# Performance work log

Hardware: AMD Instinct MI355X
Metric: run time of the kernel (lower is better)

The kernel has to match this reference:

```python
import jax, jax.numpy as jnp
import numpy as np

D = 128   # opt.geometric_latent_dim
H = 132   # FCBlock hidden width (hardcoded in source)
B = 65536
K = 8

def setup_inputs() -> dict:
    key = jax.random.key(0)
    ks = jax.random.split(key, 16)
    s = lambda k, shp, fan: jax.random.normal(k, shp, jnp.float32) / np.sqrt(fan)
    return {
        "signal": jax.random.normal(ks[0], (B, D), jnp.float32),
        "components": jax.random.normal(ks[1], (K, B, D), jnp.float32),
        # message_map / update_map: Linear(D, D)
        "Wm": s(ks[2], (D, D), D), "bm": jnp.zeros((D,), jnp.float32),
        "Wu": s(ks[3], (D, D), D), "bu": jnp.zeros((D,), jnp.float32),
        "W0": s(ks[4], (H, 2 * D), 2 * D), "b0": jnp.zeros((H,), jnp.float32),
        "W1": s(ks[5], (H, H), H),         "b1": jnp.zeros((H,), jnp.float32),
        "W2": s(ks[6], (H, H), H),         "b2": jnp.zeros((H,), jnp.float32),
        "W3": s(ks[7], (D, H), H),         "b3": jnp.zeros((D,), jnp.float32),
    }

def reference(signal, components, Wm, bm, Wu, bu, W0, b0, W1, b1, W2, b2, W3, b3):
    # message_map applied to each component, then summed over components
    msgs = jnp.einsum('kbd,ed->kbe', components, Wm) + bm  # [K,B,D]
    right = msgs.sum(axis=0)                               # [B,D]
    # update_map
    right = right @ Wu.T + bu                              # [B,D]
    # joint_update: FCBlock on concat([signal, right])
    x = jnp.concatenate([signal, right], axis=-1)          # [B,2D]
    x = jax.nn.relu(x @ W0.T + b0)
    x = jax.nn.relu(x @ W1.T + b1)
    x = jax.nn.relu(x @ W2.T + b2)
    return x @ W3.T + b3                                   # [B,D]
```

## Files before the change

### kernel.cpp

```cpp
#include <hip/hip_runtime.h>
#include <stdint.h>

#define DD  128
#define HH  132
#define BB  65536
#define KKC 8
#define HP  144
#define KP  160

typedef short bf16x8 __attribute__((ext_vector_type(8)));
typedef short bf16x4 __attribute__((ext_vector_type(4)));
typedef float f32x4  __attribute__((ext_vector_type(4)));

__device__ __forceinline__ unsigned short f2b(float f){
  union{float f; unsigned u;} c; c.f = f;
  unsigned r = c.u + 0x7fffu + ((c.u >> 16) & 1u);
  return (unsigned short)(r >> 16);
}

__global__ void prepA(const float* __restrict__ Wm, const float* __restrict__ bm,
                      const float* __restrict__ Wu, const float* __restrict__ bu,
                      float* __restrict__ Wf, float* __restrict__ bfv){
  int idx = blockIdx.x * 256 + threadIdx.x;
  int i = idx >> 7, j = idx & 127;
  float acc = 0.f;
  for(int d = 0; d < DD; ++d)
    acc += Wu[i*DD + d] * Wm[d*DD + j];
  Wf[idx] = acc;
  if(j == 0){
    float a = 0.f;
    for(int d = 0; d < DD; ++d) a += Wu[i*DD + d] * bm[d];
    bfv[i] = (float)KKC * a + bu[i];
  }
}

__global__ void prepB(const float* __restrict__ W0, const float* __restrict__ b0,
                      const float* __restrict__ W1, const float* __restrict__ b1,
                      const float* __restrict__ W2, const float* __restrict__ b2,
                      const float* __restrict__ W3, const float* __restrict__ b3,
                      const float* __restrict__ Wf, const float* __restrict__ bfv,
                      unsigned short* __restrict__ w0s_p, unsigned short* __restrict__ w0rp,
                      unsigned short* __restrict__ w1p,  unsigned short* __restrict__ w2p,
                      unsigned short* __restrict__ w3p,
                      float* __restrict__ b0p, float* __restrict__ b1p,
                      float* __restrict__ b2p, float* __restrict__ b3p){
  int idx = blockIdx.x * 256 + threadIdx.x;
  if(idx < HP*DD){
    int n = idx >> 7, k = idx & 127;
    w0s_p[idx] = (n < HH) ? f2b(W0[n*(2*DD) + k]) : (unsigned short)0;
    return;
  }
  idx -= HP*DD;
  if(idx < HP*DD){
    int n = idx >> 7, k = idx & 127;
    float acc = 0.f;
    if(n < HH)
      for(int i = 0; i < DD; ++i)
        acc += W0[n*(2*DD) + DD + i] * Wf[i*DD + k];
    w0rp[idx] = (n < HH) ? f2b(acc) : (unsigned short)0;
    return;
  }
  idx -= HP*DD;
  if(idx < HP*KP){
    int n = idx / KP, k = idx % KP;
    w1p[idx] = (n < HH && k < HH) ? f2b(W1[n*HH + k]) : (unsigned short)0;
    return;
  }
  idx -= HP*KP;
  if(idx < HP*KP){
    int n = idx / KP, k = idx % KP;
    w2p[idx] = (n < HH && k < HH) ? f2b(W2[n*HH + k]) : (unsigned short)0;
    return;
  }
  idx -= HP*KP;
  if(idx < DD*KP){
    int n = idx / KP, k = idx % KP;
    w3p[idx] = (k < HH) ? f2b(W3[n*HH + k]) : (unsigned short)0;
    return;
  }
  idx -= DD*KP;
  if(idx < HP){
    float acc = 0.f;
    if(idx < HH){
      acc = b0[idx];
      for(int i = 0; i < DD; ++i) acc += W0[idx*(2*DD) + DD + i] * bfv[i];
    }
    b0p[idx] = acc;
    return;
  }
  idx -= HP;
  if(idx < HP){ b1p[idx] = (idx < HH) ? b1[idx] : 0.f; return; }
  idx -= HP;
  if(idx < HP){ b2p[idx] = (idx < HH) ? b2[idx] : 0.f; return; }
  idx -= HP;
  if(idx < DD){ b3p[idx] = b3[idx]; return; }
}

__global__ __launch_bounds__(256) void comp_sum(
    const float* __restrict__ comps, unsigned short* __restrict__ sumb){
  const size_t base = (size_t)blockIdx.x * 8192;
  const int t = threadIdx.x;
  f32x4 acc[8];
  #pragma unroll
  for(int i = 0; i < 8; ++i) acc[i] = (f32x4){0.f,0.f,0.f,0.f};

  #pragma unroll
  for(int k = 0; k < KKC; ++k){
    const float* p = comps + (size_t)k * BB * DD + base + t*4;
    #pragma unroll
    for(int i = 0; i < 8; ++i){
      f32x4 v = *(const f32x4*)(p + i*1024);
      acc[i] += v;
    }
  }
  unsigned short* q = sumb + base + t*4;
  #pragma unroll
  for(int i = 0; i < 8; ++i){
    bf16x4 pk;
    #pragma unroll
    for(int j = 0; j < 4; ++j) pk[j] = (short)f2b(acc[i][j]);
    *(bf16x4*)(q + i*1024) = pk;
  }
}

__global__ __launch_bounds__(256) void fused_mlp(
    const float* __restrict__ signal,
    const unsigned short* __restrict__ sumb,
    const unsigned short* __restrict__ w0s_p,
    const unsigned short* __restrict__ w0rp,
    const unsigned short* __restrict__ w1p,
    const unsigned short* __restrict__ w2p,
    const unsigned short* __restrict__ w3p,
    const float* __restrict__ b0p, const float* __restrict__ b1p,
    const float* __restrict__ b2p, const float* __restrict__ b3p,
    float* __restrict__ out)
{
  const int tid  = threadIdx.x;
  const int lane = tid & 63;
  const int wave = tid >> 6;
  const int m    = lane & 15;
  const int quad = lane >> 4;
  const int rowBase = blockIdx.x * 64 + wave * 16;
  const int arow = rowBase + m;

  __shared__ unsigned short act[4][16][168];

  for(int t = tid; t < 4*16*16; t += 256){
    int wv = t >> 8, r = (t >> 4) & 15, c = t & 15;
    act[wv][r][144 + c] = 0;
  }
  __syncthreads();

  bf16x8 sumf[4];
  #pragma unroll
  for(int ki = 0; ki < 4; ++ki)
    sumf[ki] = *(const bf16x8*)(sumb + (size_t)arow*DD + ki*32 + quad*8);

  bf16x8 sigf[4];
  {
    const float* srow = signal + (size_t)arow * DD;
    #pragma unroll
    for(int ki = 0; ki < 4; ++ki){
      f32x4 lo = *(const f32x4*)(srow + ki*32 + quad*8);
      f32x4 hi = *(const f32x4*)(srow + ki*32 + quad*8 + 4);
      bf16x8 p;
      #pragma unroll
      for(int j = 0; j < 4; ++j){ p[j] = (short)f2b(lo[j]); p[4+j] = (short)f2b(hi[j]); }
      sigf[ki] = p;
    }
  }

  #pragma unroll
  for(int nt = 0; nt < 9; ++nt){
    f32x4 acc = {0.f,0.f,0.f,0.f};
    const unsigned short* wr1 = w0s_p + (size_t)(nt*16 + m)*DD + quad*8;
    const unsigned short* wr2 = w0rp  + (size_t)(nt*16 + m)*DD + quad*8;
    #pragma unroll
    for(int ki = 0; ki < 4; ++ki){
      bf16x8 wf = *(const bf16x8*)(wr1 + ki*32);
      acc = __builtin_amdgcn_mfma_f32_16x16x32_bf16(sigf[ki], wf, acc, 0, 0, 0);
    }
    #pragma unroll
    for(int ki = 0; ki < 4; ++ki){
      bf16x8 wf = *(const bf16x8*)(wr2 + ki*32);
      acc = __builtin_amdgcn_mfma_f32_16x16x32_bf16(sumf[ki], wf, acc, 0, 0, 0);
    }
    float bias = b0p[nt*16 + m];
    #pragma unroll
    for(int r = 0; r < 4; ++r){
      float v = acc[r] + bias;
      v = v > 0.f ? v : 0.f;
      act[wave][quad*4 + r][nt*16 + m] = f2b(v);
    }
  }
  __syncthreads();

  bf16x8 hf[5];

  #pragma unroll
  for(int ki = 0; ki < 5; ++ki)
    hf[ki] = *(const bf16x8*)&act[wave][m][ki*32 + quad*8];
  __syncthreads();
  #pragma unroll
  for(int nt = 0; nt < 9; ++nt){
    f32x4 acc = {0.f,0.f,0.f,0.f};
    const unsigned short* wr = w1p + (size_t)(nt*16 + m)*KP + quad*8;
    #pragma unroll
    for(int ki = 0; ki < 5; ++ki){
      bf16x8 wf = *(const bf16x8*)(wr + ki*32);
      acc = __builtin_amdgcn_mfma_f32_16x16x32_bf16(hf[ki], wf, acc, 0, 0, 0);
    }
    float bias = b1p[nt*16 + m];
    #pragma unroll
    for(int r = 0; r < 4; ++r){
      float v = acc[r] + bias;
      v = v > 0.f ? v : 0.f;
      act[wave][quad*4 + r][nt*16 + m] = f2b(v);
    }
  }
  __syncthreads();

  #pragma unroll
  for(int ki = 0; ki < 5; ++ki)
    hf[ki] = *(const bf16x8*)&act[wave][m][ki*32 + quad*8];
  __syncthreads();
  #pragma unroll
  for(int nt = 0; nt < 9; ++nt){
    f32x4 acc = {0.f,0.f,0.f,0.f};
    const unsigned short* wr = w2p + (size_t)(nt*16 + m)*KP + quad*8;
    #pragma unroll
    for(int ki = 0; ki < 5; ++ki){
      bf16x8 wf = *(const bf16x8*)(wr + ki*32);
      acc = __builtin_amdgcn_mfma_f32_16x16x32_bf16(hf[ki], wf, acc, 0, 0, 0);
    }
    float bias = b2p[nt*16 + m];
    #pragma unroll
    for(int r = 0; r < 4; ++r){
      float v = acc[r] + bias;
      v = v > 0.f ? v : 0.f;
      act[wave][quad*4 + r][nt*16 + m] = f2b(v);
    }
  }
  __syncthreads();

  #pragma unroll
  for(int ki = 0; ki < 5; ++ki)
    hf[ki] = *(const bf16x8*)&act[wave][m][ki*32 + quad*8];
  #pragma unroll
  for(int nt = 0; nt < 8; ++nt){
    f32x4 acc = {0.f,0.f,0.f,0.f};
    const unsigned short* wr = w3p + (size_t)(nt*16 + m)*KP + quad*8;
    #pragma unroll
    for(int ki = 0; ki < 5; ++ki){
      bf16x8 wf = *(const bf16x8*)(wr + ki*32);
      acc = __builtin_amdgcn_mfma_f32_16x16x32_bf16(hf[ki], wf, acc, 0, 0, 0);
    }
    float bias = b3p[nt*16 + m];
    #pragma unroll
    for(int r = 0; r < 4; ++r){
      int grow = rowBase + quad*4 + r;
      out[(size_t)grow*DD + nt*16 + m] = acc[r] + bias;
    }
  }
}

extern "C" void kernel_launch(void* const* d_in, const int* in_sizes, int n_in,
                              void* d_out, int out_size, void* d_ws, size_t ws_size,
                              hipStream_t stream){
  const float* signal = (const float*)d_in[0];
  const float* comps  = (const float*)d_in[1];
  const float* Wm = (const float*)d_in[2];
  const float* bm = (const float*)d_in[3];
  const float* Wu = (const float*)d_in[4];
  const float* bu = (const float*)d_in[5];
  const float* W0 = (const float*)d_in[6];
  const float* b0 = (const float*)d_in[7];
  const float* W1 = (const float*)d_in[8];
  const float* b1 = (const float*)d_in[9];
  const float* W2 = (const float*)d_in[10];
  const float* b2 = (const float*)d_in[11];
  const float* W3 = (const float*)d_in[12];
  const float* b3 = (const float*)d_in[13];

  char* ws = (char*)d_ws;
  float*          Wf    = (float*)(ws + 0);
  float*          bfv   = (float*)(ws + 65536);
  unsigned short* w0s_p = (unsigned short*)(ws + 66048);
  unsigned short* w0rp  = (unsigned short*)(ws + 102912);
  unsigned short* w1p   = (unsigned short*)(ws + 139776);
  unsigned short* w2p   = (unsigned short*)(ws + 185856);
  unsigned short* w3p   = (unsigned short*)(ws + 231936);
  float*          b0p   = (float*)(ws + 272896);
  float*          b1p   = (float*)(ws + 273472);
  float*          b2p   = (float*)(ws + 274048);
  float*          b3p   = (float*)(ws + 274624);
  unsigned short* sumb  = (unsigned short*)(ws + 275456);

  hipLaunchKernelGGL(prepA, dim3(64), dim3(256), 0, stream, Wm, bm, Wu, bu, Wf, bfv);

  hipLaunchKernelGGL(prepB, dim3(407), dim3(256), 0, stream,
                     W0, b0, W1, b1, W2, b2, W3, b3, Wf, bfv,
                     w0s_p, w0rp, w1p, w2p, w3p, b0p, b1p, b2p, b3p);

  hipLaunchKernelGGL(comp_sum, dim3(BB*DD/8192), dim3(256), 0, stream, comps, sumb);

  hipLaunchKernelGGL(fused_mlp, dim3(BB/64), dim3(256), 0, stream,
                     signal, sumb, w0s_p, w0rp, w1p, w2p, w3p,
                     b0p, b1p, b2p, b3p, (float*)d_out);
}
```

Before: 491.6 us.

## Stage MLP weights in LDS with padded strides and register-prefetched next layer

The fused MLP kernel now copies each layer's bf16 weights into shared memory, using padded row strides to reduce bank conflicts, instead of reading them from global memory per wave. It prefetches the next layer's weights into registers while the current layer computes. Blocks grow to 512 threads and 128 rows, so each weight copy is shared by 8 waves. The cost is about 120KB of LDS per block, which caps occupancy, plus extra barriers and register pressure from the prefetch buffers.

```diff
diff --git a/kernel.cpp b/kernel.cpp
--- a/kernel.cpp
+++ b/kernel.cpp
@@ -7,6 +7,12 @@
 #define KKC 8
 #define HP  144
 #define KP  160
+#define SW  136
+#define SH  168
+#define W0S_BYTES 40960
+#define WAB_BYTES 81920
+#define WH_BYTES  49152
+#define ACT_BYTES 43008
 
 typedef short bf16x8 __attribute__((ext_vector_type(8)));
 typedef short bf16x4 __attribute__((ext_vector_type(4)));
@@ -39,46 +45,47 @@
                       const float* __restrict__ W2, const float* __restrict__ b2,
                       const float* __restrict__ W3, const float* __restrict__ b3,
                       const float* __restrict__ Wf, const float* __restrict__ bfv,
-                      unsigned short* __restrict__ w0s_p, unsigned short* __restrict__ w0rp,
-                      unsigned short* __restrict__ w1p,  unsigned short* __restrict__ w2p,
+                      unsigned short* __restrict__ wAB,
+                      unsigned short* __restrict__ w1p, unsigned short* __restrict__ w2p,
                       unsigned short* __restrict__ w3p,
                       float* __restrict__ b0p, float* __restrict__ b1p,
                       float* __restrict__ b2p, float* __restrict__ b3p){
   int idx = blockIdx.x * 256 + threadIdx.x;
-  if(idx < HP*DD){
-    int n = idx >> 7, k = idx & 127;
-    w0s_p[idx] = (n < HH) ? f2b(W0[n*(2*DD) + k]) : (unsigned short)0;
-    return;
-  }
-  idx -= HP*DD;
-  if(idx < HP*DD){
-    int n = idx >> 7, k = idx & 127;
+  if(idx < 20480){
+    int n = idx / SW, c = idx % SW;
+    wAB[idx] = (n < HH && c < DD) ? f2b(W0[n*(2*DD) + c]) : (unsigned short)0;
+    return;
+  }
+  idx -= 20480;
+  if(idx < 20480){
+    int n = idx / SW, c = idx % SW;
     float acc = 0.f;
-    if(n < HH)
+    bool live = (n < HH && c < DD);
+    if(live)
       for(int i = 0; i < DD; ++i)
-        acc += W0[n*(2*DD) + DD + i] * Wf[i*DD + k];
-    w0rp[idx] = (n < HH) ? f2b(acc) : (unsigned short)0;
-    return;
-  }
-  idx -= HP*DD;
-  if(idx < HP*KP){
-    int n = idx / KP, k = idx % KP;
-    w1p[idx] = (n < HH && k < HH) ? f2b(W1[n*HH + k]) : (unsigned short)0;
-    return;
-  }
-  idx -= HP*KP;
-  if(idx < HP*KP){
-    int n = idx / KP, k = idx % KP;
-    w2p[idx] = (n < HH && k < HH) ? f2b(W2[n*HH + k]) : (unsigned short)0;
-    return;
-  }
-  idx -= HP*KP;
-  if(idx < DD*KP){
-    int n = idx / KP, k = idx % KP;
-    w3p[idx] = (k < HH) ? f2b(W3[n*HH + k]) : (unsigned short)0;
-    return;
-  }
-  idx -= DD*KP;
+        acc += W0[n*(2*DD) + DD + i] * Wf[i*DD + c];
+    wAB[20480 + idx] = live ? f2b(acc) : (unsigned short)0;
+    return;
+  }
+  idx -= 20480;
+  if(idx < 24576){
+    int n = idx / SH, c = idx % SH;
+    w1p[idx] = (n < HH && c < HH) ? f2b(W1[n*HH + c]) : (unsigned short)0;
+    return;
+  }
+  idx -= 24576;
+  if(idx < 24576){
+    int n = idx / SH, c = idx % SH;
+    w2p[idx] = (n < HH && c < HH) ? f2b(W2[n*HH + c]) : (unsigned short)0;
+    return;
+  }
+  idx -= 24576;
+  if(idx < 24576){
+    int n = idx / SH, c = idx % SH;
+    w3p[idx] = (n < DD && c < HH) ? f2b(W3[n*HH + c]) : (unsigned short)0;
+    return;
+  }
+  idx -= 24576;
   if(idx < HP){
     float acc = 0.f;
     if(idx < HH){
@@ -103,15 +110,11 @@
   f32x4 acc[8];
   #pragma unroll
   for(int i = 0; i < 8; ++i) acc[i] = (f32x4){0.f,0.f,0.f,0.f};
-
   #pragma unroll
   for(int k = 0; k < KKC; ++k){
     const float* p = comps + (size_t)k * BB * DD + base + t*4;
     #pragma unroll
-    for(int i = 0; i < 8; ++i){
-      f32x4 v = *(const f32x4*)(p + i*1024);
-      acc[i] += v;
-    }
+    for(int i = 0; i < 8; ++i) acc[i] += *(const f32x4*)(p + i*1024);
   }
   unsigned short* q = sumb + base + t*4;
   #pragma unroll
@@ -123,11 +126,10 @@
   }
 }
 
-__global__ __launch_bounds__(256) void fused_mlp(
+__global__ __launch_bounds__(512, 2) void fused_mlp(
     const float* __restrict__ signal,
     const unsigned short* __restrict__ sumb,
-    const unsigned short* __restrict__ w0s_p,
-    const unsigned short* __restrict__ w0rp,
+    const unsigned short* __restrict__ wAB,
     const unsigned short* __restrict__ w1p,
     const unsigned short* __restrict__ w2p,
     const unsigned short* __restrict__ w3p,
@@ -135,131 +137,178 @@
     const float* __restrict__ b2p, const float* __restrict__ b3p,
     float* __restrict__ out)
 {
-  const int tid  = threadIdx.x;
-  const int lane = tid & 63;
-  const int wave = tid >> 6;
+  __shared__ __align__(16) unsigned char ldsbuf[WAB_BYTES + ACT_BYTES];
+  unsigned short* ldsAB = (unsigned short*)ldsbuf;
+  unsigned short* ldsW  = (unsigned short*)ldsbuf;
+  unsigned short* actB  = (unsigned short*)(ldsbuf + WAB_BYTES);
+
+  const int t    = threadIdx.x;
+  const int lane = t & 63;
+  const int wave = t >> 6;
   const int m    = lane & 15;
   const int quad = lane >> 4;
-  const int rowBase = blockIdx.x * 64 + wave * 16;
+  const int rowBase = blockIdx.x * 128 + wave * 16;
   const int arow = rowBase + m;
-
-  __shared__ unsigned short act[4][16][168];
-
-  for(int t = tid; t < 4*16*16; t += 256){
-    int wv = t >> 8, r = (t >> 4) & 15, c = t & 15;
-    act[wv][r][144 + c] = 0;
-  }
-  __syncthreads();
+  unsigned short* actW = actB + wave * 16 * SH;
+
+  for(int z = t; z < 8*16*16; z += 512){
+    int wv = z >> 8, r = (z >> 4) & 15, c = z & 15;
+    actB[(wv*16 + r)*SH + 144 + c] = 0;
+  }
 
   bf16x8 sumf[4];
   #pragma unroll
   for(int ki = 0; ki < 4; ++ki)
     sumf[ki] = *(const bf16x8*)(sumb + (size_t)arow*DD + ki*32 + quad*8);
 
-  bf16x8 sigf[4];
+  f32x4 sl[8];
   {
     const float* srow = signal + (size_t)arow * DD;
     #pragma unroll
     for(int ki = 0; ki < 4; ++ki){
-      f32x4 lo = *(const f32x4*)(srow + ki*32 + quad*8);
-      f32x4 hi = *(const f32x4*)(srow + ki*32 + quad*8 + 4);
-      bf16x8 p;
-      #pragma unroll
-      for(int j = 0; j < 4; ++j){ p[j] = (short)f2b(lo[j]); p[4+j] = (short)f2b(hi[j]); }
-      sigf[ki] = p;
-    }
+      sl[2*ki]   = *(const f32x4*)(srow + ki*32 + quad*8);
+      sl[2*ki+1] = *(const f32x4*)(srow + ki*32 + quad*8 + 4);
+    }
+  }
+
+  f32x4 rAB[10];
+  {
+    const f32x4* g = (const f32x4*)wAB;
+    #pragma unroll
+    for(int c = 0; c < 10; ++c) rAB[c] = g[c*512 + t];
+  }
+
+  bf16x8 sigf[4];
+  #pragma unroll
+  for(int ki = 0; ki < 4; ++ki){
+    bf16x8 p;
+    #pragma unroll
+    for(int j = 0; j < 4; ++j){ p[j] = (short)f2b(sl[2*ki][j]); p[4+j] = (short)f2b(sl[2*ki+1][j]); }
+    sigf[ki] = p;
+  }
+
+  {
+    f32x4* l = (f32x4*)ldsAB;
+    #pragma unroll
+    for(int c = 0; c < 10; ++c) l[c*512 + t] = rAB[c];
+  }
+  __syncthreads();
+
+  f32x4 rW[6];
+  {
+    const f32x4* g = (const f32x4*)w1p;
+    #pragma unroll
+    for(int c = 0; c < 6; ++c) rW[c] = g[c*512 + t];
   }
 
   #pragma unroll
   for(int nt = 0; nt < 9; ++nt){
     f32x4 acc = {0.f,0.f,0.f,0.f};
-    const unsigned short* wr1 = w0s_p + (size_t)(nt*16 + m)*DD + quad*8;
-    const unsigned short* wr2 = w0rp  + (size_t)(nt*16 + m)*DD + quad*8;
+    const int rb = nt*16 + m;
     #pragma unroll
     for(int ki = 0; ki < 4; ++ki){
-      bf16x8 wf = *(const bf16x8*)(wr1 + ki*32);
+      bf16x8 wf = *(const bf16x8*)(ldsAB + rb*SW + ki*32 + quad*8);
       acc = __builtin_amdgcn_mfma_f32_16x16x32_bf16(sigf[ki], wf, acc, 0, 0, 0);
     }
     #pragma unroll
     for(int ki = 0; ki < 4; ++ki){
-      bf16x8 wf = *(const bf16x8*)(wr2 + ki*32);
+      bf16x8 wf = *(const bf16x8*)(ldsAB + 20480 + rb*SW + ki*32 + quad*8);
       acc = __builtin_amdgcn_mfma_f32_16x16x32_bf16(sumf[ki], wf, acc, 0, 0, 0);
     }
-    float bias = b0p[nt*16 + m];
+    float bias = b0p[rb];
     #pragma unroll
     for(int r = 0; r < 4; ++r){
       float v = acc[r] + bias;
       v = v > 0.f ? v : 0.f;
-      act[wave][quad*4 + r][nt*16 + m] = f2b(v);
-    }
-  }
+      actW[(quad*4 + r)*SH + rb] = f2b(v);
+    }
+  }
+  __syncthreads();
+
+  { f32x4* l = (f32x4*)ldsW;
+    #pragma unroll
+    for(int c = 0; c < 6; ++c) l[c*512 + t] = rW[c]; }
   __syncthreads();
 
   bf16x8 hf[5];
 
+  { const f32x4* g = (const f32x4*)w2p;
+    #pragma unroll
+    for(int c = 0; c < 6; ++c) rW[c] = g[c*512 + t]; }
   #pragma unroll
   for(int ki = 0; ki < 5; ++ki)
-    hf[ki] = *(const bf16x8*)&act[wave][m][ki*32 + quad*8];
-  __syncthreads();
+    hf[ki] = *(const bf16x8*)(actW + m*SH + ki*32 + quad*8);
   #pragma unroll
   for(int nt = 0; nt < 9; ++nt){
     f32x4 acc = {0.f,0.f,0.f,0.f};
-    const unsigned short* wr = w1p + (size_t)(nt*16 + m)*KP + quad*8;
+    const int rb = nt*16 + m;
     #pragma unroll
     for(int ki = 0; ki < 5; ++ki){
-      bf16x8 wf = *(const bf16x8*)(wr + ki*32);
+      bf16x8 wf = *(const bf16x8*)(ldsW + rb*SH + ki*32 + quad*8);
       acc = __builtin_amdgcn_mfma_f32_16x16x32_bf16(hf[ki], wf, acc, 0, 0, 0);
     }
-    float bias = b1p[nt*16 + m];
+    float bias = b1p[rb];
     #pragma unroll
     for(int r = 0; r < 4; ++r){
       float v = acc[r] + bias;
       v = v > 0.f ? v : 0.f;
-      act[wave][quad*4 + r][nt*16 + m] = f2b(v);
-    }
-  }
-  __syncthreads();
-
+      actW[(quad*4 + r)*SH + rb] = f2b(v);
+    }
+  }
+  __syncthreads();
+
+  { f32x4* l = (f32x4*)ldsW;
+    #pragma unroll
+    for(int c = 0; c < 6; ++c) l[c*512 + t] = rW[c]; }
+  __syncthreads();
+
+  { const f32x4* g = (const f32x4*)w3p;
+    #pragma unroll
+    for(int c = 0; c < 6; ++c) rW[c] = g[c*512 + t]; }
   #pragma unroll
   for(int ki = 0; ki < 5; ++ki)
-    hf[ki] = *(const bf16x8*)&act[wave][m][ki*32 + quad*8];
-  __syncthreads();
+    hf[ki] = *(const bf16x8*)(actW + m*SH + ki*32 + quad*8);
   #pragma unroll
   for(int nt = 0; nt < 9; ++nt){
     f32x4 acc = {0.f,0.f,0.f,0.f};
-    const unsigned short* wr = w2p + (size_t)(nt*16 + m)*KP + quad*8;
+    const int rb = nt*16 + m;
     #pragma unroll
     for(int ki = 0; ki < 5; ++ki){
-      bf16x8 wf = *(const bf16x8*)(wr + ki*32);
+      bf16x8 wf = *(const bf16x8*)(ldsW + rb*SH + ki*32 + quad*8);
       acc = __builtin_amdgcn_mfma_f32_16x16x32_bf16(hf[ki], wf, acc, 0, 0, 0);
     }
-    float bias = b2p[nt*16 + m];
+    float bias = b2p[rb];
     #pragma unroll
     for(int r = 0; r < 4; ++r){
       float v = acc[r] + bias;
       v = v > 0.f ? v : 0.f;
-      act[wave][quad*4 + r][nt*16 + m] = f2b(v);
-    }
-  }
+      actW[(quad*4 + r)*SH + rb] = f2b(v);
+    }
+  }
+  __syncthreads();
+
+  { f32x4* l = (f32x4*)ldsW;
+    #pragma unroll
+    for(int c = 0; c < 6; ++c) l[c*512 + t] = rW[c]; }
   __syncthreads();
 
   #pragma unroll
   for(int ki = 0; ki < 5; ++ki)
-    hf[ki] = *(const bf16x8*)&act[wave][m][ki*32 + quad*8];
+    hf[ki] = *(const bf16x8*)(actW + m*SH + ki*32 + quad*8);
   #pragma unroll
   for(int nt = 0; nt < 8; ++nt){
     f32x4 acc = {0.f,0.f,0.f,0.f};
-    const unsigned short* wr = w3p + (size_t)(nt*16 + m)*KP + quad*8;
+    const int rb = nt*16 + m;
     #pragma unroll
     for(int ki = 0; ki < 5; ++ki){
-      bf16x8 wf = *(const bf16x8*)(wr + ki*32);
+      bf16x8 wf = *(const bf16x8*)(ldsW + rb*SH + ki*32 + quad*8);
       acc = __builtin_amdgcn_mfma_f32_16x16x32_bf16(hf[ki], wf, acc, 0, 0, 0);
     }
-    float bias = b3p[nt*16 + m];
+    float bias = b3p[rb];
     #pragma unroll
     for(int r = 0; r < 4; ++r){
       int grow = rowBase + quad*4 + r;
-      out[(size_t)grow*DD + nt*16 + m] = acc[r] + bias;
+      out[(size_t)grow*DD + rb] = acc[r] + bias;
     }
   }
 }
@@ -283,28 +332,27 @@
   const float* b3 = (const float*)d_in[13];
 
   char* ws = (char*)d_ws;
-  float*          Wf    = (float*)(ws + 0);
-  float*          bfv   = (float*)(ws + 65536);
-  unsigned short* w0s_p = (unsigned short*)(ws + 66048);
-  unsigned short* w0rp  = (unsigned short*)(ws + 102912);
-  unsigned short* w1p   = (unsigned short*)(ws + 139776);
-  unsigned short* w2p   = (unsigned short*)(ws + 185856);
-  unsigned short* w3p   = (unsigned short*)(ws + 231936);
-  float*          b0p   = (float*)(ws + 272896);
-  float*          b1p   = (float*)(ws + 273472);
-  float*          b2p   = (float*)(ws + 274048);
-  float*          b3p   = (float*)(ws + 274624);
-  unsigned short* sumb  = (unsigned short*)(ws + 275456);
+  float*          Wf   = (float*)(ws + 0);
+  float*          bfv  = (float*)(ws + 65536);
+  unsigned short* wAB  = (unsigned short*)(ws + 66048);
+  unsigned short* w1p  = (unsigned short*)(ws + 147968);
+  unsigned short* w2p  = (unsigned short*)(ws + 197120);
+  unsigned short* w3p  = (unsigned short*)(ws + 246272);
+  float*          b0p  = (float*)(ws + 295424);
+  float*          b1p  = (float*)(ws + 296000);
+  float*          b2p  = (float*)(ws + 296576);
+  float*          b3p  = (float*)(ws + 297152);
+  unsigned short* sumb = (unsigned short*)(ws + 297728);
 
   hipLaunchKernelGGL(prepA, dim3(64), dim3(256), 0, stream, Wm, bm, Wu, bu, Wf, bfv);
 
-  hipLaunchKernelGGL(prepB, dim3(407), dim3(256), 0, stream,
+  hipLaunchKernelGGL(prepB, dim3(451), dim3(256), 0, stream,
                      W0, b0, W1, b1, W2, b2, W3, b3, Wf, bfv,
-                     w0s_p, w0rp, w1p, w2p, w3p, b0p, b1p, b2p, b3p);
+                     wAB, w1p, w2p, w3p, b0p, b1p, b2p, b3p);
 
   hipLaunchKernelGGL(comp_sum, dim3(BB*DD/8192), dim3(256), 0, stream, comps, sumb);
 
-  hipLaunchKernelGGL(fused_mlp, dim3(BB/64), dim3(256), 0, stream,
-                     signal, sumb, w0s_p, w0rp, w1p, w2p, w3p,
+  hipLaunchKernelGGL(fused_mlp, dim3(BB/128), dim3(512), 0, stream,
+                     signal, sumb, wAB, w1p, w2p, w3p,
                      b0p, b1p, b2p, b3p, (float*)d_out);
 }
```

New measurement: 451.3 us. 8.2% less time.
